# Performance work log

Hardware: AMD Instinct MI355X
Metric: run time of the kernel (lower is better)

Reference implementation:

```python
import jax, jax.numpy as jnp
import numpy as np

G, NI, EI = 10000, 32, 128        # inner graphs, nodes/graph, edges/graph
EO = 160000                        # outer edges
F_IN, H, F_G, NC = 64, 128, 128, 32


def gcn_conv(h, src, dst, n_nodes, W, b):
    # DGL GraphConv, norm='both': D^-1/2 A D^-1/2 h W + b (degree from dst)
    deg = jax.ops.segment_sum(jnp.ones(src.shape[0], h.dtype), dst, num_segments=n_nodes)
    norm = jnp.where(deg > 0, deg, 1.0) ** -0.5
    msg = h[src] * norm[src, None]                       # [E, F]
    agg = jax.ops.segment_sum(msg, dst, num_segments=n_nodes) * norm[:, None]
    return agg @ W + b


def gcn_stack(h, src, dst, n_nodes, params):
    n = len(params)
    for i, (W, b) in enumerate(params):
        h = gcn_conv(h, src, dst, n_nodes, W, b)
        if i < n - 1:
            h = jax.nn.relu(h)
    return h


def setup_inputs() -> dict:
    key = jax.random.key(0)
    ks = jax.random.split(key, 20)
    inp = {
        'inner_features': jax.random.normal(ks[0], (G, NI, F_IN), jnp.float32),
        'inner_src': jax.random.randint(ks[1], (G, EI), 0, NI, jnp.int32),
        'inner_dst': jax.random.randint(ks[2], (G, EI), 0, NI, jnp.int32),
        'outer_src': jax.random.randint(ks[3], (EO,), 0, G, jnp.int32),
        'outer_dst': jax.random.randint(ks[4], (EO,), 0, G, jnp.int32),
    }
    def lin(k, fi, fo):
        s = 1.0 / np.sqrt(fi)
        return jax.random.uniform(k, (fi, fo), jnp.float32, -s, s)
    # inner GCN: F_IN -> H -> H -> F_G
    inp['Wi0'], inp['bi0'] = lin(ks[5], F_IN, H), jnp.zeros((H,), jnp.float32)
    inp['Wi1'], inp['bi1'] = lin(ks[6], H, H), jnp.zeros((H,), jnp.float32)
    inp['Wi2'], inp['bi2'] = lin(ks[7], H, F_G), jnp.zeros((F_G,), jnp.float32)
    # outer GCN: F_G -> H -> H -> NC
    inp['Wo0'], inp['bo0'] = lin(ks[8], F_G, H), jnp.zeros((H,), jnp.float32)
    inp['Wo1'], inp['bo1'] = lin(ks[9], H, H), jnp.zeros((H,), jnp.float32)
    inp['Wo2'], inp['bo2'] = lin(ks[10], H, NC), jnp.zeros((NC,), jnp.float32)
    return inp


def reference(inner_features, inner_src, inner_dst, outer_src, outer_dst,
              Wi0, bi0, Wi1, bi1, Wi2, bi2, Wo0, bo0, Wo1, bo1, Wo2, bo2):
    inner_params = [(Wi0, bi0), (Wi1, bi1), (Wi2, bi2)]
    outer_params = [(Wo0, bo0), (Wo1, bo1), (Wo2, bo2)]
    # vectorized replacement for the per-inner-graph Python loop
    h_inner = jax.vmap(lambda h, s, d: gcn_stack(h, s, d, NI, inner_params))(
        inner_features, inner_src, inner_dst)          # [G, NI, F_G]
    features_new = jnp.mean(h_inner, axis=1)           # torch.mean(h, dim=0) per graph -> [G, F_G]
    return gcn_stack(features_new, outer_src, outer_dst, G, outer_params)  # [G, NC]
```

## Files before the change

### kernel.cpp

```cpp
#include <hip/hip_runtime.h>
#include <math.h>


constexpr int G_N  = 10000;
constexpr int NI_N = 32;
constexpr int EI_N = 128;
constexpr int EO_N = 160000;
constexpr int FIN  = 64;
constexpr int HD   = 128;
constexpr int NCLS = 32;

typedef short bf16x8 __attribute__((ext_vector_type(8)));
typedef float f32x4  __attribute__((ext_vector_type(4)));

#define MFMA16(a, b, c) __builtin_amdgcn_mfma_f32_16x16x32_bf16((a), (b), (c), 0, 0, 0)

__device__ __forceinline__ unsigned short f2bf(float x) {
  unsigned int u = __builtin_bit_cast(unsigned int, x);
  u += 0x7fffu + ((u >> 16) & 1u);
  return (unsigned short)(u >> 16);
}

__global__ __launch_bounds__(256) void pack_all_w(
    const float* __restrict__ W0, const float* __restrict__ W1,
    const float* __restrict__ W2, short* __restrict__ o0,
    short* __restrict__ o1, short* __restrict__ o2) {
  const int b = blockIdx.x;
  const float* W; short* out; int K, idx;
  if (b < 4)       { W = W0; out = o0; K = 64;  idx = b * 256 + threadIdx.x; }
  else if (b < 12) { W = W1; out = o1; K = 128; idx = (b - 4) * 256 + threadIdx.x; }
  else             { W = W2; out = o2; K = 128; idx = (b - 12) * 256 + threadIdx.x; }
  const int KB = K >> 5;
  const int lane = idx & 63;
  const int ctkb = idx >> 6;
  const int kb = ctkb % KB;
  const int ct = ctkb / KB;
  const int col = 16 * ct + (lane & 15);
  const int k0 = 32 * kb + 8 * (lane >> 4);
#pragma unroll
  for (int j = 0; j < 8; ++j)
    out[idx * 8 + j] = (short)f2bf(W[(k0 + j) * HD + col]);
}

template <int NCT, bool RELU, bool LAST>
__device__ __forceinline__ void gcn_layer_w(
    int l, const short* __restrict__ sMp, short* __restrict__ sH,
    short* __restrict__ sT, const short* __restrict__ Wp,
    const float* __restrict__ bias, float* __restrict__ outp) {
  constexpr int KB = NCT / 2;
  const int lg = l >> 4, c15 = l & 15, jj = l & 7;
  const f32x4 z = {0.f, 0.f, 0.f, 0.f};

#pragma unroll
  for (int rt = 0; rt < 2; ++rt) {
    const bf16x8 am = *(const bf16x8*)&sMp[(rt * 64 + l) * 8];
#pragma unroll
    for (int ct = 0; ct < NCT; ++ct) {
      const bf16x8 bh = *(const bf16x8*)&sH[(ct * 64 + l) * 8];
      f32x4 d = MFMA16(am, bh, z);
      const int kb = ct >> 1;
      const int hi = ((ct & 1) << 1) | (c15 >> 3);
      const int base = ((rt * 4 + kb) * 64 + 16 * hi + 4 * lg) * 8 + jj;
#pragma unroll
      for (int r = 0; r < 4; ++r) sT[base + r * 8] = (short)f2bf(d[r]);
    }
  }

  bf16x8 a0[KB], a1[KB];
#pragma unroll
  for (int kb = 0; kb < KB; ++kb) {
    a0[kb] = *(const bf16x8*)&sT[((0 + kb) * 64 + l) * 8];
    a1[kb] = *(const bf16x8*)&sT[((4 + kb) * 64 + l) * 8];
  }
  float pool[8];
#pragma unroll
  for (int ct2 = 0; ct2 < 8; ++ct2) {
    f32x4 acc0 = z, acc1 = z;
#pragma unroll
    for (int kb = 0; kb < KB; ++kb) {
      const bf16x8 bw = *(const bf16x8*)&Wp[((ct2 * KB + kb) * 64 + l) * 8];
      acc0 = MFMA16(a0[kb], bw, acc0);
      acc1 = MFMA16(a1[kb], bw, acc1);
    }
    const float bv = bias[16 * ct2 + c15];
    if (LAST) {
      pool[ct2] = (acc0[0] + acc0[1] + acc0[2] + acc0[3]) +
                  (acc1[0] + acc1[1] + acc1[2] + acc1[3]) + 8.f * bv;
    } else {
      {
        float v0 = acc0[0] + bv, v1 = acc0[1] + bv, v2 = acc0[2] + bv, v3 = acc0[3] + bv;
        if (RELU) { v0 = fmaxf(v0, 0.f); v1 = fmaxf(v1, 0.f);
                    v2 = fmaxf(v2, 0.f); v3 = fmaxf(v3, 0.f); }
        const ushort4 pk = make_ushort4(f2bf(v0), f2bf(v1), f2bf(v2), f2bf(v3));
        const int g2 = (lg >> 1);
        *(ushort4*)&sH[(ct2 * 64 + c15 + 16 * g2) * 8 + 4 * (lg & 1)] = pk;
      }
      {
        float v0 = acc1[0] + bv, v1 = acc1[1] + bv, v2 = acc1[2] + bv, v3 = acc1[3] + bv;
        if (RELU) { v0 = fmaxf(v0, 0.f); v1 = fmaxf(v1, 0.f);
                    v2 = fmaxf(v2, 0.f); v3 = fmaxf(v3, 0.f); }
        const ushort4 pk = make_ushort4(f2bf(v0), f2bf(v1), f2bf(v2), f2bf(v3));
        const int g2 = 2 + (lg >> 1);
        *(ushort4*)&sH[(ct2 * 64 + c15 + 16 * g2) * 8 + 4 * (lg & 1)] = pk;
      }
    }
  }
  if (LAST) {
#pragma unroll
    for (int ct2 = 0; ct2 < 8; ++ct2) {
      float p = pool[ct2];
      p += __shfl_xor(p, 16);
      p += __shfl_xor(p, 32);
      if (l < 16) outp[16 * ct2 + c15] = p * (1.0f / NI_N);
    }
  }
}

__global__ __launch_bounds__(64) void inner_gcn_kernel(
    const float* __restrict__ feats, const int* __restrict__ src,
    const int* __restrict__ dst,
    const short* __restrict__ wp0, const float* __restrict__ bi0,
    const short* __restrict__ wp1, const float* __restrict__ bi1,
    const short* __restrict__ wp2, const float* __restrict__ bi2,
    float* __restrict__ feat_out) {
  __shared__ __align__(16) short sH[8 * 64 * 8];
  __shared__ __align__(16) short sT[8 * 64 * 8];
  __shared__ __align__(16) short sMp[2 * 64 * 8];
  __shared__ float sNorm[NI_N];

  const int l = threadIdx.x;
  const int gid = blockIdx.x;
  const int lg = l >> 4, c15 = l & 15;
  float* sMf = (float*)sT;

  const float4* f4 = (const float4*)(feats + (size_t)gid * (NI_N * FIN));
  float4 hv[8];
#pragma unroll
  for (int it = 0; it < 8; ++it) hv[it] = f4[it * 64 + l];

  const int2 es = ((const int2*)(src + gid * EI_N))[l];
  const int2 ed = ((const int2*)(dst + gid * EI_N))[l];

#pragma unroll
  for (int i = 0; i < 18; ++i) sMf[i * 64 + l] = 0.f;
  atomicAdd(&sMf[ed.x * 36 + es.x], 1.0f);
  atomicAdd(&sMf[ed.y * 36 + es.y], 1.0f);

  {
    const int row = l & 31;
    const float* pr = &sMf[row * 36 + (l >> 5) * 16];
    const float4 q0 = *(const float4*)(pr + 0);
    const float4 q1 = *(const float4*)(pr + 4);
    const float4 q2 = *(const float4*)(pr + 8);
    const float4 q3 = *(const float4*)(pr + 12);
    float p = (q0.x + q0.y + q0.z + q0.w) + (q1.x + q1.y + q1.z + q1.w) +
              (q2.x + q2.y + q2.z + q2.w) + (q3.x + q3.y + q3.z + q3.w);
    p += __shfl_xor(p, 32);
    if (l < 32) sNorm[l] = (p > 0.f) ? (1.0f / sqrtf(p)) : 1.0f;
  }

  {
    const int k0 = 8 * lg;
    const float4 n0 = *(const float4*)&sNorm[k0];
    const float4 n1 = *(const float4*)&sNorm[k0 + 4];
#pragma unroll
    for (int rb = 0; rb < 2; ++rb) {
      const int row = 16 * rb + c15;
      const float nr = sNorm[row];
      const float4 a = *(const float4*)&sMf[row * 36 + k0];
      const float4 b = *(const float4*)&sMf[row * 36 + k0 + 4];
      bf16x8 o;
      o[0] = (short)f2bf(a.x * nr * n0.x); o[1] = (short)f2bf(a.y * nr * n0.y);
      o[2] = (short)f2bf(a.z * nr * n0.z); o[3] = (short)f2bf(a.w * nr * n0.w);
      o[4] = (short)f2bf(b.x * nr * n1.x); o[5] = (short)f2bf(b.y * nr * n1.y);
      o[6] = (short)f2bf(b.z * nr * n1.z); o[7] = (short)f2bf(b.w * nr * n1.w);
      *(bf16x8*)&sMp[(rb * 64 + l) * 8] = o;
    }
  }

#pragma unroll
  for (int it = 0; it < 8; ++it) {
    const int n = it * 4 + lg;
    const int ct = c15 >> 2;
    const int c0 = (c15 & 3) * 4;
    const int lanebase = 16 * (n >> 3);
    const int jj = n & 7;
    const float4 v = hv[it];
    sH[(ct * 64 + c0 + 0 + lanebase) * 8 + jj] = (short)f2bf(v.x);
    sH[(ct * 64 + c0 + 1 + lanebase) * 8 + jj] = (short)f2bf(v.y);
    sH[(ct * 64 + c0 + 2 + lanebase) * 8 + jj] = (short)f2bf(v.z);
    sH[(ct * 64 + c0 + 3 + lanebase) * 8 + jj] = (short)f2bf(v.w);
  }

  gcn_layer_w<4, true, false>(l, sMp, sH, sT, wp0, bi0, nullptr);
  gcn_layer_w<8, true, false>(l, sMp, sH, sT, wp1, bi1, nullptr);
  gcn_layer_w<8, false, true>(l, sMp, sH, sT, wp2, bi2,
                              feat_out + (size_t)gid * HD);
}

__global__ __launch_bounds__(256) void hist_kernel(const int* __restrict__ dst,
                                                   int* __restrict__ degi) {
  const int e = blockIdx.x * 256 + threadIdx.x;
  if (e < EO_N) atomicAdd(&degi[dst[e]], 1);
}

__global__ __launch_bounds__(1024) void scan_norm_kernel(
    const int* __restrict__ degi, int* __restrict__ start,
    int* __restrict__ cursor, float* __restrict__ nrm) {
  __shared__ int part[1024];
  const int t = threadIdx.x;
  const int base = t * 10;
  int loc[10];
  int s = 0;
#pragma unroll
  for (int k = 0; k < 10; ++k) {
    const int i = base + k;
    const int d = (i < G_N) ? degi[i] : 0;
    loc[k] = s;
    s += d;
  }
  part[t] = s;
  __syncthreads();
  for (int off = 1; off < 1024; off <<= 1) {
    const int v = (t >= off) ? part[t - off] : 0;
    __syncthreads();
    part[t] += v;
    __syncthreads();
  }
  const int excl = (t == 0) ? 0 : part[t - 1];
#pragma unroll
  for (int k = 0; k < 10; ++k) {
    const int i = base + k;
    if (i < G_N) {
      const int st = excl + loc[k];
      start[i] = st;
      cursor[i] = st;
      const int d = degi[i];
      nrm[i] = (d > 0) ? (1.0f / sqrtf((float)d)) : 1.0f;
    }
  }
}

__global__ __launch_bounds__(256) void fill_kernel(const int* __restrict__ src,
                                                   const int* __restrict__ dst,
                                                   int* __restrict__ cursor,
                                                   int* __restrict__ esrc) {
  const int e = blockIdx.x * 256 + threadIdx.x;
  if (e < EO_N) {
    const int pos = atomicAdd(&cursor[dst[e]], 1);
    esrc[pos] = src[e];
  }
}

template <int Nout, bool RELU>
__global__ __launch_bounds__(256) void gather_mm_kernel(
    const float* __restrict__ h, const int* __restrict__ esrc,
    const int* __restrict__ start, const int* __restrict__ degi,
    const float* __restrict__ nrm, const float* __restrict__ W,
    const float* __restrict__ bias, float* __restrict__ out) {
  __shared__ __align__(16) float sIn[16 * HD];
  const int t = threadIdx.x;
  const int row0 = blockIdx.x * 16;
  const int rr = t >> 4, sub = t & 15;
  const int ehalf = sub >> 3, fq = sub & 7;
  const int row = row0 + rr;
  float4 a0 = {0,0,0,0}, a1 = {0,0,0,0}, a2 = {0,0,0,0}, a3 = {0,0,0,0};
  {
    const int s0 = start[row];
    const int cnt = degi[row];
    const float* hb = h + (size_t)fq * 16;
    for (int i = ehalf; i < cnt; i += 2) {
      const int s = esrc[s0 + i];
      const float ns = nrm[s];
      const float* p = hb + (size_t)s * HD;
      const float4 v0 = *(const float4*)(p + 0);
      const float4 v1 = *(const float4*)(p + 4);
      const float4 v2 = *(const float4*)(p + 8);
      const float4 v3 = *(const float4*)(p + 12);
      a0.x = fmaf(v0.x, ns, a0.x); a0.y = fmaf(v0.y, ns, a0.y);
      a0.z = fmaf(v0.z, ns, a0.z); a0.w = fmaf(v0.w, ns, a0.w);
      a1.x = fmaf(v1.x, ns, a1.x); a1.y = fmaf(v1.y, ns, a1.y);
      a1.z = fmaf(v1.z, ns, a1.z); a1.w = fmaf(v1.w, ns, a1.w);
      a2.x = fmaf(v2.x, ns, a2.x); a2.y = fmaf(v2.y, ns, a2.y);
      a2.z = fmaf(v2.z, ns, a2.z); a2.w = fmaf(v2.w, ns, a2.w);
      a3.x = fmaf(v3.x, ns, a3.x); a3.y = fmaf(v3.y, ns, a3.y);
      a3.z = fmaf(v3.z, ns, a3.z); a3.w = fmaf(v3.w, ns, a3.w);
    }
  }
  float* q = &sIn[rr * HD + fq * 16];
  if (ehalf == 0) {
    *(float4*)(q + 0) = a0; *(float4*)(q + 4) = a1;
    *(float4*)(q + 8) = a2; *(float4*)(q + 12) = a3;
  }
  __syncthreads();
  if (ehalf == 1) {
    const float nr = nrm[row];
    float4 b0 = *(const float4*)(q + 0), b1 = *(const float4*)(q + 4);
    float4 b2 = *(const float4*)(q + 8), b3 = *(const float4*)(q + 12);
    b0.x = (b0.x + a0.x) * nr; b0.y = (b0.y + a0.y) * nr;
    b0.z = (b0.z + a0.z) * nr; b0.w = (b0.w + a0.w) * nr;
    b1.x = (b1.x + a1.x) * nr; b1.y = (b1.y + a1.y) * nr;
    b1.z = (b1.z + a1.z) * nr; b1.w = (b1.w + a1.w) * nr;
    b2.x = (b2.x + a2.x) * nr; b2.y = (b2.y + a2.y) * nr;
    b2.z = (b2.z + a2.z) * nr; b2.w = (b2.w + a2.w) * nr;
    b3.x = (b3.x + a3.x) * nr; b3.y = (b3.y + a3.y) * nr;
    b3.z = (b3.z + a3.z) * nr; b3.w = (b3.w + a3.w) * nr;
    *(float4*)(q + 0) = b0; *(float4*)(q + 4) = b1;
    *(float4*)(q + 8) = b2; *(float4*)(q + 12) = b3;
  }
  __syncthreads();
  constexpr int NC4 = Nout / 4;
  constexpr int TILES = 4 * NC4;
  if (t < TILES) {
    const int r = t / NC4, c = t % NC4;
    float acc[4][4] = {};
#pragma unroll 8
    for (int k = 0; k < HD; ++k) {
      const float4 wv = *(const float4*)&W[k * Nout + c * 4];
      const float a0s = sIn[(r * 4 + 0) * HD + k];
      const float a1s = sIn[(r * 4 + 1) * HD + k];
      const float a2s = sIn[(r * 4 + 2) * HD + k];
      const float a3s = sIn[(r * 4 + 3) * HD + k];
      acc[0][0] = fmaf(a0s, wv.x, acc[0][0]);
      acc[0][1] = fmaf(a0s, wv.y, acc[0][1]);
      acc[0][2] = fmaf(a0s, wv.z, acc[0][2]);
      acc[0][3] = fmaf(a0s, wv.w, acc[0][3]);
      acc[1][0] = fmaf(a1s, wv.x, acc[1][0]);
      acc[1][1] = fmaf(a1s, wv.y, acc[1][1]);
      acc[1][2] = fmaf(a1s, wv.z, acc[1][2]);
      acc[1][3] = fmaf(a1s, wv.w, acc[1][3]);
      acc[2][0] = fmaf(a2s, wv.x, acc[2][0]);
      acc[2][1] = fmaf(a2s, wv.y, acc[2][1]);
      acc[2][2] = fmaf(a2s, wv.z, acc[2][2]);
      acc[2][3] = fmaf(a2s, wv.w, acc[2][3]);
      acc[3][0] = fmaf(a3s, wv.x, acc[3][0]);
      acc[3][1] = fmaf(a3s, wv.y, acc[3][1]);
      acc[3][2] = fmaf(a3s, wv.z, acc[3][2]);
      acc[3][3] = fmaf(a3s, wv.w, acc[3][3]);
    }
    const float4 bv = *(const float4*)&bias[c * 4];
#pragma unroll
    for (int i = 0; i < 4; ++i) {
      float4 v = make_float4(acc[i][0] + bv.x, acc[i][1] + bv.y,
                             acc[i][2] + bv.z, acc[i][3] + bv.w);
      if (RELU) {
        v.x = fmaxf(v.x, 0.f); v.y = fmaxf(v.y, 0.f);
        v.z = fmaxf(v.z, 0.f); v.w = fmaxf(v.w, 0.f);
      }
      *(float4*)&out[(size_t)(row0 + r * 4 + i) * Nout + c * 4] = v;
    }
  }
}

extern "C" void kernel_launch(void* const* d_in, const int* in_sizes, int n_in,
                              void* d_out, int out_size, void* d_ws,
                              size_t ws_size, hipStream_t stream) {
  const float* feats = (const float*)d_in[0];
  const int* isrc = (const int*)d_in[1];
  const int* idst = (const int*)d_in[2];
  const int* osrc = (const int*)d_in[3];
  const int* odst = (const int*)d_in[4];
  const float* Wi0 = (const float*)d_in[5];
  const float* bi0 = (const float*)d_in[6];
  const float* Wi1 = (const float*)d_in[7];
  const float* bi1 = (const float*)d_in[8];
  const float* Wi2 = (const float*)d_in[9];
  const float* bi2 = (const float*)d_in[10];
  const float* Wo0 = (const float*)d_in[11];
  const float* bo0 = (const float*)d_in[12];
  const float* Wo1 = (const float*)d_in[13];
  const float* bo1 = (const float*)d_in[14];
  const float* Wo2 = (const float*)d_in[15];
  const float* bo2 = (const float*)d_in[16];
  float* out = (float*)d_out;

  float* ws = (float*)d_ws;
  float* feat = ws;
  float* h0   = ws + (size_t)G_N * HD;
  float* nrm  = ws + (size_t)3 * G_N * HD;
  int* degi   = (int*)(ws + (size_t)3 * G_N * HD + G_N);
  int* start  = degi + G_N;
  int* cursor = start + G_N;
  int* esrc   = cursor + G_N;
  short* wp0  = (short*)(esrc + EO_N);
  short* wp1  = wp0 + 8 * 2 * 64 * 8;
  short* wp2  = wp1 + 8 * 4 * 64 * 8;

  pack_all_w<<<20, 256, 0, stream>>>(Wi0, Wi1, Wi2, wp0, wp1, wp2);

  inner_gcn_kernel<<<G_N, 64, 0, stream>>>(feats, isrc, idst, wp0, bi0, wp1,
                                           bi1, wp2, bi2, feat);

  hipMemsetAsync(degi, 0, G_N * sizeof(int), stream);
  hist_kernel<<<(EO_N + 255) / 256, 256, 0, stream>>>(odst, degi);
  scan_norm_kernel<<<1, 1024, 0, stream>>>(degi, start, cursor, nrm);
  fill_kernel<<<(EO_N + 255) / 256, 256, 0, stream>>>(osrc, odst, cursor, esrc);

  const int gm_grid = G_N / 16;
  gather_mm_kernel<HD, true><<<gm_grid, 256, 0, stream>>>(
      feat, esrc, start, degi, nrm, Wo0, bo0, h0);
  gather_mm_kernel<HD, true><<<gm_grid, 256, 0, stream>>>(
      h0, esrc, start, degi, nrm, Wo1, bo1, feat);
  gather_mm_kernel<NCLS, false><<<gm_grid, 256, 0, stream>>>(
      feat, esrc, start, degi, nrm, Wo2, bo2, out);
}
```

Before: 179.7 us.

## Keep inner GCN operands in registers and rebalance outer gather-matmul parallelism

The inner GCN kernel now keeps the normalized adjacency fragments and the node feature fragments in registers instead of shared memory. This drops the sH and sMp buffers, cutting LDS use per block, and adds a launch-bounds occupancy hint. The outer gather-matmul kernel is templated on rows per block and edge split: the hidden layers use 8 rows with a 4-way edge split, and the matmul gives each thread one row instead of a 4x4 tile. This spreads work over more threads and blocks, at the cost of less register reuse of W and more register pressure in the inner kernel.

```diff
diff --git a/kernel.cpp b/kernel.cpp
--- a/kernel.cpp
+++ b/kernel.cpp
@@ -43,21 +43,19 @@
 }
 
 template <int NCT, bool RELU, bool LAST>
-__device__ __forceinline__ void gcn_layer_w(
-    int l, const short* __restrict__ sMp, short* __restrict__ sH,
-    short* __restrict__ sT, const short* __restrict__ Wp,
-    const float* __restrict__ bias, float* __restrict__ outp) {
+__device__ __forceinline__ void gcn_layer_r(
+    int l, const bf16x8 am[2], bf16x8 hreg[8], short* __restrict__ sT,
+    const short* __restrict__ Wp, const float* __restrict__ bias,
+    float* __restrict__ outp) {
   constexpr int KB = NCT / 2;
   const int lg = l >> 4, c15 = l & 15, jj = l & 7;
   const f32x4 z = {0.f, 0.f, 0.f, 0.f};
 
 #pragma unroll
   for (int rt = 0; rt < 2; ++rt) {
-    const bf16x8 am = *(const bf16x8*)&sMp[(rt * 64 + l) * 8];
 #pragma unroll
     for (int ct = 0; ct < NCT; ++ct) {
-      const bf16x8 bh = *(const bf16x8*)&sH[(ct * 64 + l) * 8];
-      f32x4 d = MFMA16(am, bh, z);
+      f32x4 d = MFMA16(am[rt], hreg[ct], z);
       const int kb = ct >> 1;
       const int hi = ((ct & 1) << 1) | (c15 >> 3);
       const int base = ((rt * 4 + kb) * 64 + 16 * hi + 4 * lg) * 8 + jj;
@@ -93,7 +91,7 @@
                     v2 = fmaxf(v2, 0.f); v3 = fmaxf(v3, 0.f); }
         const ushort4 pk = make_ushort4(f2bf(v0), f2bf(v1), f2bf(v2), f2bf(v3));
         const int g2 = (lg >> 1);
-        *(ushort4*)&sH[(ct2 * 64 + c15 + 16 * g2) * 8 + 4 * (lg & 1)] = pk;
+        *(ushort4*)&sT[(ct2 * 64 + c15 + 16 * g2) * 8 + 4 * (lg & 1)] = pk;
       }
       {
         float v0 = acc1[0] + bv, v1 = acc1[1] + bv, v2 = acc1[2] + bv, v3 = acc1[3] + bv;
@@ -101,7 +99,7 @@
                     v2 = fmaxf(v2, 0.f); v3 = fmaxf(v3, 0.f); }
         const ushort4 pk = make_ushort4(f2bf(v0), f2bf(v1), f2bf(v2), f2bf(v3));
         const int g2 = 2 + (lg >> 1);
-        *(ushort4*)&sH[(ct2 * 64 + c15 + 16 * g2) * 8 + 4 * (lg & 1)] = pk;
+        *(ushort4*)&sT[(ct2 * 64 + c15 + 16 * g2) * 8 + 4 * (lg & 1)] = pk;
       }
     }
   }
@@ -113,20 +111,22 @@
       p += __shfl_xor(p, 32);
       if (l < 16) outp[16 * ct2 + c15] = p * (1.0f / NI_N);
     }
-  }
-}
-
-__global__ __launch_bounds__(64) void inner_gcn_kernel(
+  } else {
+#pragma unroll
+    for (int ct = 0; ct < 8; ++ct)
+      hreg[ct] = *(const bf16x8*)&sT[(ct * 64 + l) * 8];
+  }
+}
+
+__global__ __launch_bounds__(64, 4) void inner_gcn_kernel(
     const float* __restrict__ feats, const int* __restrict__ src,
     const int* __restrict__ dst,
     const short* __restrict__ wp0, const float* __restrict__ bi0,
     const short* __restrict__ wp1, const float* __restrict__ bi1,
     const short* __restrict__ wp2, const float* __restrict__ bi2,
     float* __restrict__ feat_out) {
-  __shared__ __align__(16) short sH[8 * 64 * 8];
   __shared__ __align__(16) short sT[8 * 64 * 8];
-  __shared__ __align__(16) short sMp[2 * 64 * 8];
-  __shared__ float sNorm[NI_N];
+  __shared__ __align__(16) float sNorm[NI_N];
 
   const int l = threadIdx.x;
   const int gid = blockIdx.x;
@@ -159,6 +159,7 @@
     if (l < 32) sNorm[l] = (p > 0.f) ? (1.0f / sqrtf(p)) : 1.0f;
   }
 
+  bf16x8 am[2];
   {
     const int k0 = 8 * lg;
     const float4 n0 = *(const float4*)&sNorm[k0];
@@ -174,9 +175,10 @@
       o[2] = (short)f2bf(a.z * nr * n0.z); o[3] = (short)f2bf(a.w * nr * n0.w);
       o[4] = (short)f2bf(b.x * nr * n1.x); o[5] = (short)f2bf(b.y * nr * n1.y);
       o[6] = (short)f2bf(b.z * nr * n1.z); o[7] = (short)f2bf(b.w * nr * n1.w);
-      *(bf16x8*)&sMp[(rb * 64 + l) * 8] = o;
-    }
-  }
+      am[rb] = o;
+    }
+  }
+  __syncthreads();
 
 #pragma unroll
   for (int it = 0; it < 8; ++it) {
@@ -186,15 +188,19 @@
     const int lanebase = 16 * (n >> 3);
     const int jj = n & 7;
     const float4 v = hv[it];
-    sH[(ct * 64 + c0 + 0 + lanebase) * 8 + jj] = (short)f2bf(v.x);
-    sH[(ct * 64 + c0 + 1 + lanebase) * 8 + jj] = (short)f2bf(v.y);
-    sH[(ct * 64 + c0 + 2 + lanebase) * 8 + jj] = (short)f2bf(v.z);
-    sH[(ct * 64 + c0 + 3 + lanebase) * 8 + jj] = (short)f2bf(v.w);
-  }
-
-  gcn_layer_w<4, true, false>(l, sMp, sH, sT, wp0, bi0, nullptr);
-  gcn_layer_w<8, true, false>(l, sMp, sH, sT, wp1, bi1, nullptr);
-  gcn_layer_w<8, false, true>(l, sMp, sH, sT, wp2, bi2,
+    sT[(ct * 64 + c0 + 0 + lanebase) * 8 + jj] = (short)f2bf(v.x);
+    sT[(ct * 64 + c0 + 1 + lanebase) * 8 + jj] = (short)f2bf(v.y);
+    sT[(ct * 64 + c0 + 2 + lanebase) * 8 + jj] = (short)f2bf(v.z);
+    sT[(ct * 64 + c0 + 3 + lanebase) * 8 + jj] = (short)f2bf(v.w);
+  }
+  bf16x8 hreg[8];
+#pragma unroll
+  for (int ct = 0; ct < 4; ++ct)
+    hreg[ct] = *(const bf16x8*)&sT[(ct * 64 + l) * 8];
+
+  gcn_layer_r<4, true, false>(l, am, hreg, sT, wp0, bi0, nullptr);
+  gcn_layer_r<8, true, false>(l, am, hreg, sT, wp1, bi1, nullptr);
+  gcn_layer_r<8, false, true>(l, am, hreg, sT, wp2, bi2,
                               feat_out + (size_t)gid * HD);
 }
 
@@ -252,16 +258,18 @@
   }
 }
 
-template <int Nout, bool RELU>
+template <int ROWS, int ESPL, int Nout, bool RELU>
 __global__ __launch_bounds__(256) void gather_mm_kernel(
     const float* __restrict__ h, const int* __restrict__ esrc,
     const int* __restrict__ start, const int* __restrict__ degi,
     const float* __restrict__ nrm, const float* __restrict__ W,
     const float* __restrict__ bias, float* __restrict__ out) {
-  __shared__ __align__(16) float sIn[16 * HD];
+  constexpr int TPR = 256 / ROWS;
+  __shared__ __align__(16) float sIn[ROWS * HD];
+  __shared__ __align__(16) float sPart[(ESPL - 1) * ROWS * HD + 1];
   const int t = threadIdx.x;
-  const int row0 = blockIdx.x * 16;
-  const int rr = t >> 4, sub = t & 15;
+  const int row0 = blockIdx.x * ROWS;
+  const int rr = t / TPR, sub = t % TPR;
   const int ehalf = sub >> 3, fq = sub & 7;
   const int row = row0 + rr;
   float4 a0 = {0,0,0,0}, a1 = {0,0,0,0}, a2 = {0,0,0,0}, a3 = {0,0,0,0};
@@ -269,7 +277,7 @@
     const int s0 = start[row];
     const int cnt = degi[row];
     const float* hb = h + (size_t)fq * 16;
-    for (int i = ehalf; i < cnt; i += 2) {
+    for (int i = ehalf; i < cnt; i += ESPL) {
       const int s = esrc[s0 + i];
       const float ns = nrm[s];
       const float* p = hb + (size_t)s * HD;
@@ -287,68 +295,53 @@
       a3.z = fmaf(v3.z, ns, a3.z); a3.w = fmaf(v3.w, ns, a3.w);
     }
   }
-  float* q = &sIn[rr * HD + fq * 16];
-  if (ehalf == 0) {
+  if (ehalf > 0) {
+    float* q = &sPart[((ehalf - 1) * ROWS + rr) * HD + fq * 16];
     *(float4*)(q + 0) = a0; *(float4*)(q + 4) = a1;
     *(float4*)(q + 8) = a2; *(float4*)(q + 12) = a3;
   }
   __syncthreads();
-  if (ehalf == 1) {
+  if (ehalf == 0) {
     const float nr = nrm[row];
-    float4 b0 = *(const float4*)(q + 0), b1 = *(const float4*)(q + 4);
-    float4 b2 = *(const float4*)(q + 8), b3 = *(const float4*)(q + 12);
-    b0.x = (b0.x + a0.x) * nr; b0.y = (b0.y + a0.y) * nr;
-    b0.z = (b0.z + a0.z) * nr; b0.w = (b0.w + a0.w) * nr;
-    b1.x = (b1.x + a1.x) * nr; b1.y = (b1.y + a1.y) * nr;
-    b1.z = (b1.z + a1.z) * nr; b1.w = (b1.w + a1.w) * nr;
-    b2.x = (b2.x + a2.x) * nr; b2.y = (b2.y + a2.y) * nr;
-    b2.z = (b2.z + a2.z) * nr; b2.w = (b2.w + a2.w) * nr;
-    b3.x = (b3.x + a3.x) * nr; b3.y = (b3.y + a3.y) * nr;
-    b3.z = (b3.z + a3.z) * nr; b3.w = (b3.w + a3.w) * nr;
-    *(float4*)(q + 0) = b0; *(float4*)(q + 4) = b1;
-    *(float4*)(q + 8) = b2; *(float4*)(q + 12) = b3;
+#pragma unroll
+    for (int e = 1; e < ESPL; ++e) {
+      const float* q = &sPart[((e - 1) * ROWS + rr) * HD + fq * 16];
+      const float4 b0 = *(const float4*)(q + 0), b1 = *(const float4*)(q + 4);
+      const float4 b2 = *(const float4*)(q + 8), b3 = *(const float4*)(q + 12);
+      a0.x += b0.x; a0.y += b0.y; a0.z += b0.z; a0.w += b0.w;
+      a1.x += b1.x; a1.y += b1.y; a1.z += b1.z; a1.w += b1.w;
+      a2.x += b2.x; a2.y += b2.y; a2.z += b2.z; a2.w += b2.w;
+      a3.x += b3.x; a3.y += b3.y; a3.z += b3.z; a3.w += b3.w;
+    }
+    a0.x *= nr; a0.y *= nr; a0.z *= nr; a0.w *= nr;
+    a1.x *= nr; a1.y *= nr; a1.z *= nr; a1.w *= nr;
+    a2.x *= nr; a2.y *= nr; a2.z *= nr; a2.w *= nr;
+    a3.x *= nr; a3.y *= nr; a3.z *= nr; a3.w *= nr;
+    float* q = &sIn[rr * HD + fq * 16];
+    *(float4*)(q + 0) = a0; *(float4*)(q + 4) = a1;
+    *(float4*)(q + 8) = a2; *(float4*)(q + 12) = a3;
   }
   __syncthreads();
   constexpr int NC4 = Nout / 4;
-  constexpr int TILES = 4 * NC4;
-  if (t < TILES) {
-    const int r = t / NC4, c = t % NC4;
-    float acc[4][4] = {};
+  const int r = t / NC4, c = t % NC4;
+  if (r < ROWS) {
+    float acc0 = 0.f, acc1 = 0.f, acc2 = 0.f, acc3 = 0.f;
 #pragma unroll 8
     for (int k = 0; k < HD; ++k) {
       const float4 wv = *(const float4*)&W[k * Nout + c * 4];
-      const float a0s = sIn[(r * 4 + 0) * HD + k];
-      const float a1s = sIn[(r * 4 + 1) * HD + k];
-      const float a2s = sIn[(r * 4 + 2) * HD + k];
-      const float a3s = sIn[(r * 4 + 3) * HD + k];
-      acc[0][0] = fmaf(a0s, wv.x, acc[0][0]);
-      acc[0][1] = fmaf(a0s, wv.y, acc[0][1]);
-      acc[0][2] = fmaf(a0s, wv.z, acc[0][2]);
-      acc[0][3] = fmaf(a0s, wv.w, acc[0][3]);
-      acc[1][0] = fmaf(a1s, wv.x, acc[1][0]);
-      acc[1][1] = fmaf(a1s, wv.y, acc[1][1]);
-      acc[1][2] = fmaf(a1s, wv.z, acc[1][2]);
-      acc[1][3] = fmaf(a1s, wv.w, acc[1][3]);
-      acc[2][0] = fmaf(a2s, wv.x, acc[2][0]);
-      acc[2][1] = fmaf(a2s, wv.y, acc[2][1]);
-      acc[2][2] = fmaf(a2s, wv.z, acc[2][2]);
-      acc[2][3] = fmaf(a2s, wv.w, acc[2][3]);
-      acc[3][0] = fmaf(a3s, wv.x, acc[3][0]);
-      acc[3][1] = fmaf(a3s, wv.y, acc[3][1]);
-      acc[3][2] = fmaf(a3s, wv.z, acc[3][2]);
-      acc[3][3] = fmaf(a3s, wv.w, acc[3][3]);
+      const float av = sIn[r * HD + k];
+      acc0 = fmaf(av, wv.x, acc0);
+      acc1 = fmaf(av, wv.y, acc1);
+      acc2 = fmaf(av, wv.z, acc2);
+      acc3 = fmaf(av, wv.w, acc3);
     }
     const float4 bv = *(const float4*)&bias[c * 4];
-#pragma unroll
-    for (int i = 0; i < 4; ++i) {
-      float4 v = make_float4(acc[i][0] + bv.x, acc[i][1] + bv.y,
-                             acc[i][2] + bv.z, acc[i][3] + bv.w);
-      if (RELU) {
-        v.x = fmaxf(v.x, 0.f); v.y = fmaxf(v.y, 0.f);
-        v.z = fmaxf(v.z, 0.f); v.w = fmaxf(v.w, 0.f);
-      }
-      *(float4*)&out[(size_t)(row0 + r * 4 + i) * Nout + c * 4] = v;
-    }
+    float4 v = make_float4(acc0 + bv.x, acc1 + bv.y, acc2 + bv.z, acc3 + bv.w);
+    if (RELU) {
+      v.x = fmaxf(v.x, 0.f); v.y = fmaxf(v.y, 0.f);
+      v.z = fmaxf(v.z, 0.f); v.w = fmaxf(v.w, 0.f);
+    }
+    *(float4*)&out[(size_t)(row0 + r) * Nout + c * 4] = v;
   }
 }
 
@@ -396,11 +389,10 @@
   scan_norm_kernel<<<1, 1024, 0, stream>>>(degi, start, cursor, nrm);
   fill_kernel<<<(EO_N + 255) / 256, 256, 0, stream>>>(osrc, odst, cursor, esrc);
 
-  const int gm_grid = G_N / 16;
-  gather_mm_kernel<HD, true><<<gm_grid, 256, 0, stream>>>(
+  gather_mm_kernel<8, 4, HD, true><<<G_N / 8, 256, 0, stream>>>(
       feat, esrc, start, degi, nrm, Wo0, bo0, h0);
-  gather_mm_kernel<HD, true><<<gm_grid, 256, 0, stream>>>(
+  gather_mm_kernel<8, 4, HD, true><<<G_N / 8, 256, 0, stream>>>(
       h0, esrc, start, degi, nrm, Wo1, bo1, feat);
-  gather_mm_kernel<NCLS, false><<<gm_grid, 256, 0, stream>>>(
+  gather_mm_kernel<16, 2, NCLS, false><<<G_N / 16, 256, 0, stream>>>(
       feat, esrc, start, degi, nrm, Wo2, bo2, out);
 }
```

Measured after the change: 191.8 us. 6.8% more time.
